# Kernel optimization log

Hardware: AMD Instinct MI355X
Metric: run time of the kernel (lower is better)

Reference implementation:

```python
import jax, jax.numpy as jnp
import numpy as np

LB_WEIGHT = 0.01  # load_balance_loss_weight


def setup_inputs() -> dict:
    key = jax.random.key(0)
    ks = jax.random.split(key, 5)
    B, S, D, F, E = 2, 2048, 1024, 4096, 8
    scale = 0.02
    return {
        "x": jax.random.normal(ks[0], (B, S, D), dtype=jnp.float32),
        "Wr": jax.random.normal(ks[1], (E, D), dtype=jnp.float32) * scale,
        "W1": jax.random.normal(ks[2], (E, F, D), dtype=jnp.float32) * scale,
        "b1": jnp.zeros((E, F), dtype=jnp.float32),
        "W2": jax.random.normal(ks[3], (E, D, F), dtype=jnp.float32) * scale,
        "b2": jnp.zeros((E, D), dtype=jnp.float32),
        "top_k": 2,
    }


def reference(x, Wr, W1, b1, W2, b2, top_k):
    B, S, D = x.shape
    E = Wr.shape[0]
    x_flat = x.reshape(-1, D)                      # (T, D)

    # Router: softmax over experts, then top-k with renormalized gates.
    router_logits = x_flat @ Wr.T                  # (T, E)
    router_probs = jax.nn.softmax(router_logits, axis=-1)
    topk_p, topk_idx = jax.lax.top_k(router_probs, top_k)   # (T, K)
    topk_p = topk_p / jnp.sum(topk_p, axis=-1, keepdims=True)

    # Combine weights per expert: w[t, e] = sum_k topk_p[t, k] * [idx[t, k] == e]
    one_hot = jax.nn.one_hot(topk_idx, E, dtype=x.dtype)     # (T, K, E)
    combine = jnp.einsum("tk,tke->te", topk_p, one_hot)      # (T, E)

    # Expert FFNs (dense over all experts; masked-out experts get zero weight).
    # FeedForward: Linear(D->F) -> GELU -> Linear(F->D); dropout is identity (eval).
    h = jnp.einsum("td,efd->tef", x_flat, W1) + b1           # (T, E, F)
    h = jax.nn.gelu(h)
    expert_out = jnp.einsum("tef,edf->ted", h, W2) + b2      # (T, E, D)

    out_flat = jnp.einsum("te,ted->td", combine, expert_out) # (T, D)
    output = out_flat.reshape(B, S, D)

    # Load-balance aux loss.
    expert_usage = jnp.mean(router_probs, axis=0)            # (E,)
    aux_loss = LB_WEIGHT * jnp.sum((expert_usage - 1.0 / E) ** 2)
    return output, aux_loss
```

## Files before the change

kernel.cpp:

```cpp
#include <hip/hip_runtime.h>
#include <hip/hip_bf16.h>
#include <stdint.h>

#define D_DIM 1024
#define F_DIM 4096
#define E_NUM 8
#define BM2 256
#define BN2 128
#define BK 64
#define MAXTILES 80
#define MAXT256 40

typedef __attribute__((ext_vector_type(4))) float f32x4;
typedef __attribute__((ext_vector_type(8))) short bf16x8;

#define C_CNT   0
#define C_CUR   8
#define C_OFF   16
#define C_NT    25
#define C_TE    26
#define C_TR    (26+MAXTILES)
#define C_USAGE (26+2*MAXTILES)

__device__ __forceinline__ void gload_lds16(const void* g, void* l) {
  __builtin_amdgcn_global_load_lds((const __attribute__((address_space(1))) void*)g,
                                   (__attribute__((address_space(3))) void*)l, 16, 0, 0);
}

__device__ __forceinline__ float bf2f(unsigned short u) {
  union { unsigned int i; float f; } c; c.i = ((unsigned int)u) << 16; return c.f;
}

__global__ void cvt_k(const float* __restrict__ s, unsigned short* __restrict__ d, int n4) {
  const int stride = gridDim.x * blockDim.x;
  for (int i = blockIdx.x * blockDim.x + threadIdx.x; i < n4; i += stride) {
    float4 v = ((const float4*)s)[i];
    __hip_bfloat16 h0 = __float2bfloat16(v.x);
    __hip_bfloat16 h1 = __float2bfloat16(v.y);
    __hip_bfloat16 h2 = __float2bfloat16(v.z);
    __hip_bfloat16 h3 = __float2bfloat16(v.w);
    ushort4 o;
    o.x = *(unsigned short*)&h0; o.y = *(unsigned short*)&h1;
    o.z = *(unsigned short*)&h2; o.w = *(unsigned short*)&h3;
    ((ushort4*)d)[i] = o;
  }
}

__global__ __launch_bounds__(256) void router_k(
    const float* __restrict__ x, const float* __restrict__ Wr,
    int* __restrict__ t2i, float* __restrict__ t2g,
    float* __restrict__ usage_part, unsigned short* __restrict__ xb, int T) {
  __shared__ float us[4][E_NUM];
  const int wave = threadIdx.x >> 6;
  const int lane = threadIdx.x & 63;
  const int gw = blockIdx.x * 4 + wave;
  const float4* xt = (const float4*)(x + (size_t)gw * D_DIM);
  const float4* wr4 = (const float4*)Wr;
  unsigned short* xrow = xb + (size_t)gw * D_DIM;
  float l[E_NUM] = {0.f,0.f,0.f,0.f,0.f,0.f,0.f,0.f};
#pragma unroll
  for (int it = 0; it < D_DIM / 256; it++) {
    const int i4 = it * 64 + lane;
    const float4 xv = xt[i4];
    __hip_bfloat16 c0 = __float2bfloat16(xv.x), c1 = __float2bfloat16(xv.y);
    __hip_bfloat16 c2 = __float2bfloat16(xv.z), c3 = __float2bfloat16(xv.w);
    ushort4 ov; ov.x = *(unsigned short*)&c0; ov.y = *(unsigned short*)&c1;
    ov.z = *(unsigned short*)&c2; ov.w = *(unsigned short*)&c3;
    ((ushort4*)xrow)[i4] = ov;
#pragma unroll
    for (int e = 0; e < E_NUM; e++) {
      const float4 w = wr4[e * (D_DIM / 4) + i4];
      l[e] += xv.x * w.x + xv.y * w.y + xv.z * w.z + xv.w * w.w;
    }
  }
#pragma unroll
  for (int e = 0; e < E_NUM; e++) {
    float v = l[e];
    v += __shfl_xor(v, 32); v += __shfl_xor(v, 16); v += __shfl_xor(v, 8);
    v += __shfl_xor(v, 4);  v += __shfl_xor(v, 2);  v += __shfl_xor(v, 1);
    l[e] = v;
  }
  float m = l[0];
#pragma unroll
  for (int e = 1; e < E_NUM; e++) m = fmaxf(m, l[e]);
  float p[E_NUM]; float s = 0.f;
#pragma unroll
  for (int e = 0; e < E_NUM; e++) { p[e] = expf(l[e] - m); s += p[e]; }
  const float inv = 1.0f / s;
  float v1 = l[0]; int i1 = 0;
#pragma unroll
  for (int e = 1; e < E_NUM; e++) { if (l[e] > v1) { v1 = l[e]; i1 = e; } }
  float v2 = -3.0e38f; int i2 = 0;
#pragma unroll
  for (int e = 0; e < E_NUM; e++) { if (e != i1 && l[e] > v2) { v2 = l[e]; i2 = e; } }
  const float p1 = expf(v1 - m);
  const float p2 = expf(v2 - m);
  const float gd = 1.0f / (p1 + p2);
  if (lane == 0) {
    t2i[gw * 2] = i1; t2i[gw * 2 + 1] = i2;
    t2g[gw * 2] = p1 * gd; t2g[gw * 2 + 1] = p2 * gd;
#pragma unroll
    for (int e = 0; e < E_NUM; e++) us[wave][e] = p[e] * inv;
  }
  __syncthreads();
  if (threadIdx.x < E_NUM) {
    const int e = threadIdx.x;
    usage_part[blockIdx.x * E_NUM + e] = us[0][e] + us[1][e] + us[2][e] + us[3][e];
  }
}

__global__ __launch_bounds__(256) void reduce_k(
    const float* __restrict__ usage_part, const int* __restrict__ t2i,
    int* __restrict__ ctrl, float* __restrict__ aux_out, int nblk, int T2, int T) {
  __shared__ float usum[E_NUM];
  __shared__ int hist[E_NUM];
  if (threadIdx.x < E_NUM) { usum[threadIdx.x] = 0.f; hist[threadIdx.x] = 0; }
  __syncthreads();
  {
    const int e = threadIdx.x & 7;
    const int chunk = threadIdx.x >> 3;
    float s = 0.f;
    for (int i = chunk; i < nblk; i += 32) s += usage_part[i * E_NUM + e];
    atomicAdd(&usum[e], s);
  }
  {
    int h[E_NUM] = {0,0,0,0,0,0,0,0};
    for (int i = threadIdx.x; i < T2; i += 256) h[t2i[i] & 7]++;
#pragma unroll
    for (int e = 0; e < E_NUM; e++) if (h[e]) atomicAdd(&hist[e], h[e]);
  }
  __syncthreads();
  if (threadIdx.x == 0) {
    int off = 0, nt = 0;
    float loss = 0.f;
    for (int e = 0; e < E_NUM; e++) {
      ctrl[C_CNT + e] = hist[e];
      ctrl[C_OFF + e] = off;
      ctrl[C_CUR + e] = off;
      const int c = hist[e];
      const int ntile = (c + BM2 - 1) / BM2;
      for (int i = 0; i < ntile; i++) {
        ctrl[C_TE + nt] = e;
        ctrl[C_TR + nt] = off + i * BM2;
        nt++;
      }
      off += c;
      const float um = usum[e] / (float)T - 1.0f / (float)E_NUM;
      loss += um * um;
    }
    ctrl[C_OFF + E_NUM] = off;
    ctrl[C_NT] = nt;
    aux_out[0] = 0.01f * loss;
  }
}

__global__ void scatter_k(const int* __restrict__ t2i, int* __restrict__ ctrl,
                          int* __restrict__ rmap, int* __restrict__ slots, int T) {
  const int t = blockIdx.x * blockDim.x + threadIdx.x;
  if (t >= T) return;
#pragma unroll
  for (int k = 0; k < 2; k++) {
    const int e = t2i[t * 2 + k];
    const int slot = atomicAdd(&ctrl[C_CUR + e], 1);
    rmap[slot] = t;
    slots[t * 2 + k] = slot;
  }
}


#define STAGE(K0, AL, BL)                                            \
  {                                                                  \
    _Pragma("unroll")                                                \
    for (int i = 0; i < 4; i++) gload_lds16(a_src[i] + (K0), AL[i]); \
    _Pragma("unroll")                                                \
    for (int j = 0; j < 2; j++) gload_lds16(b_src[j] + (K0), BL[j]); \
  }

#define COMPUTE(AC, BC)                                              \
  {                                                                  \
    _Pragma("unroll")                                                \
    for (int kh = 0; kh < 2; ++kh) {                                 \
      const int co = (((kh * 4 + ckq) ^ swz) << 4);                  \
      bf16x8 af[8], bfv[2];                                          \
      _Pragma("unroll")                                              \
      for (int mi = 0; mi < 8; mi++)                                 \
        af[mi] = *(const bf16x8*)((AC) + (rA + mi * 16) * 128 + co); \
      _Pragma("unroll")                                              \
      for (int ni = 0; ni < 2; ni++)                                 \
        bfv[ni] = *(const bf16x8*)((BC) + (rB + ni * 16) * 128 + co);\
      _Pragma("unroll")                                              \
      for (int mi = 0; mi < 8; mi++)                                 \
        _Pragma("unroll")                                            \
        for (int ni = 0; ni < 2; ni++)                               \
          acc[mi][ni] = __builtin_amdgcn_mfma_f32_16x16x32_bf16(af[mi], bfv[ni], acc[mi][ni], 0, 0, 0); \
    }                                                                \
  }

__global__ __launch_bounds__(512, 2) void gemm1_k(
    const unsigned short* __restrict__ xb, const unsigned short* __restrict__ W1b,
    const float* __restrict__ b1, unsigned short* __restrict__ hb,
    const int* __restrict__ rmap, const int* __restrict__ ctrl, int T2) {
  extern __shared__ char smem[];
  const int lin = blockIdx.x;
  const int lin2 = (lin & 7) * 160 + (lin >> 3);
  const int tile = lin2 >> 5;
  const int fbase = (lin2 & 31) * BN2;

  const int nt = ctrl[C_NT];
  if (tile >= nt) return;
  const int e = ctrl[C_TE + tile];
  const int rowbase = ctrl[C_TR + tile];
  const int row_end = ctrl[C_OFF + e + 1];

  const int tid = threadIdx.x;
  const int lane = tid & 63;
  const int wave = tid >> 6;

  const unsigned short* a_src[4];
  const unsigned short* b_src[2];
  char *aL0[4], *aL1[4], *bL0[2], *bL1[2];
#pragma unroll
  for (int i = 0; i < 4; i++) {
    const int c = tid + 512 * i;
    const int r = c >> 3, cc = c & 7;
    const int sc = cc ^ (r & 7);
    int pos = rowbase + r; pos = pos < T2 ? pos : T2 - 1;
    a_src[i] = xb + (size_t)rmap[pos] * D_DIM + sc * 8;
    aL0[i] = smem + c * 16;
    aL1[i] = smem + 32768 + c * 16;
  }
#pragma unroll
  for (int j = 0; j < 2; j++) {
    const int c2 = tid + 512 * j;
    const int r = c2 >> 3, cc = c2 & 7;
    const int sc = cc ^ (r & 7);
    b_src[j] = W1b + ((size_t)e * F_DIM + (size_t)(fbase + r)) * D_DIM + sc * 8;
    bL0[j] = smem + 65536 + c2 * 16;
    bL1[j] = smem + 81920 + c2 * 16;
  }
  const char* As0 = smem;          const char* As1 = smem + 32768;
  const char* Bs0 = smem + 65536;  const char* Bs1 = smem + 81920;

  f32x4 acc[8][2] = {};
  const int wm = wave >> 2, wn = wave & 3;
  const int rA = wm * 128 + (lane & 15);
  const int rB = wn * 32 + (lane & 15);
  const int swz = lane & 7;
  const int ckq = lane >> 4;

  STAGE(0, aL0, bL0);
  const int NK = D_DIM / BK;
  for (int kt = 0; kt < NK; kt += 2) {
    STAGE((kt + 1) * BK, aL1, bL1);
    asm volatile("s_waitcnt vmcnt(6)" ::: "memory");
    __builtin_amdgcn_s_barrier();
    __builtin_amdgcn_sched_barrier(0);
    COMPUTE(As0, Bs0);
    __builtin_amdgcn_sched_barrier(0);
    __builtin_amdgcn_s_barrier();
    if (kt + 2 < NK) {
      STAGE((kt + 2) * BK, aL0, bL0);
      asm volatile("s_waitcnt vmcnt(6)" ::: "memory");
    } else {
      asm volatile("s_waitcnt vmcnt(0)" ::: "memory");
    }
    __builtin_amdgcn_s_barrier();
    __builtin_amdgcn_sched_barrier(0);
    COMPUTE(As1, Bs1);
    __builtin_amdgcn_sched_barrier(0);
    __builtin_amdgcn_s_barrier();
  }

  const int r_rem = row_end - rowbase;
  const float* b1e = b1 + (size_t)e * F_DIM;
  float bias[2];
#pragma unroll
  for (int ni = 0; ni < 2; ni++)
    bias[ni] = b1e[fbase + wn * 32 + ni * 16 + (lane & 15)];
#pragma unroll
  for (int mi = 0; mi < 8; mi++) {
#pragma unroll
    for (int q = 0; q < 4; q++) {
      const int rr = wm * 128 + mi * 16 + (lane >> 4) * 4 + q;
      if (rr < r_rem) {
        unsigned short* hrow = hb + (size_t)(rowbase + rr) * F_DIM;
#pragma unroll
        for (int ni = 0; ni < 2; ni++) {
          const int col = fbase + wn * 32 + ni * 16 + (lane & 15);
          const float v = acc[mi][ni][q] + bias[ni];
          const float u2 = 1.5957691216057308f * (v + 0.044715f * v * v * v);
          const float gg = v / (1.0f + __expf(-u2));
          __hip_bfloat16 hv = __float2bfloat16(gg);
          hrow[col] = *(unsigned short*)&hv;
        }
      }
    }
  }
}

__global__ __launch_bounds__(512, 2) void gemm2_k(
    const unsigned short* __restrict__ hb, const unsigned short* __restrict__ W2b,
    unsigned short* __restrict__ y2, const int* __restrict__ ctrl, int T2) {
  extern __shared__ char smem[];
  const int lin = blockIdx.x;
  const int lin2 = (lin & 7) * 160 + (lin >> 3);
  const int tile = lin2 >> 5;
  const int rest = lin2 & 31;
  const int z = rest >> 3;
  const int dbase = (rest & 7) * BN2;

  const int nt = ctrl[C_NT];
  if (tile >= nt) return;
  const int e = ctrl[C_TE + tile];
  const int rowbase = ctrl[C_TR + tile];
  const int row_end = ctrl[C_OFF + e + 1];
  const int kt0 = z * (F_DIM / BK / 4);

  const int tid = threadIdx.x;
  const int lane = tid & 63;
  const int wave = tid >> 6;

  const unsigned short* a_src[4];
  const unsigned short* b_src[2];
  char *aL0[4], *aL1[4], *bL0[2], *bL1[2];
#pragma unroll
  for (int i = 0; i < 4; i++) {
    const int c = tid + 512 * i;
    const int r = c >> 3, cc = c & 7;
    const int sc = cc ^ (r & 7);
    int pos = rowbase + r; pos = pos < T2 ? pos : T2 - 1;
    a_src[i] = hb + (size_t)pos * F_DIM + sc * 8;
    aL0[i] = smem + c * 16;
    aL1[i] = smem + 32768 + c * 16;
  }
#pragma unroll
  for (int j = 0; j < 2; j++) {
    const int c2 = tid + 512 * j;
    const int r = c2 >> 3, cc = c2 & 7;
    const int sc = cc ^ (r & 7);
    b_src[j] = W2b + ((size_t)e * D_DIM + (size_t)(dbase + r)) * F_DIM + sc * 8;
    bL0[j] = smem + 65536 + c2 * 16;
    bL1[j] = smem + 81920 + c2 * 16;
  }
  const char* As0 = smem;          const char* As1 = smem + 32768;
  const char* Bs0 = smem + 65536;  const char* Bs1 = smem + 81920;

  f32x4 acc[8][2] = {};
  const int wm = wave >> 2, wn = wave & 3;
  const int rA = wm * 128 + (lane & 15);
  const int rB = wn * 32 + (lane & 15);
  const int swz = lane & 7;
  const int ckq = lane >> 4;

  const int NKH = F_DIM / BK / 4;
  STAGE(kt0 * BK, aL0, bL0);
  for (int kt = kt0; kt < kt0 + NKH; kt += 2) {
    STAGE((kt + 1) * BK, aL1, bL1);
    asm volatile("s_waitcnt vmcnt(6)" ::: "memory");
    __builtin_amdgcn_s_barrier();
    __builtin_amdgcn_sched_barrier(0);
    COMPUTE(As0, Bs0);
    __builtin_amdgcn_sched_barrier(0);
    __builtin_amdgcn_s_barrier();
    if (kt + 2 < kt0 + NKH) {
      STAGE((kt + 2) * BK, aL0, bL0);
      asm volatile("s_waitcnt vmcnt(6)" ::: "memory");
    } else {
      asm volatile("s_waitcnt vmcnt(0)" ::: "memory");
    }
    __builtin_amdgcn_s_barrier();
    __builtin_amdgcn_sched_barrier(0);
    COMPUTE(As1, Bs1);
    __builtin_amdgcn_sched_barrier(0);
    __builtin_amdgcn_s_barrier();
  }

  const int r_rem = row_end - rowbase;
  unsigned short* yz = y2 + (size_t)z * T2 * D_DIM;
#pragma unroll
  for (int mi = 0; mi < 8; mi++) {
#pragma unroll
    for (int q = 0; q < 4; q++) {
      const int rr = wm * 128 + mi * 16 + (lane >> 4) * 4 + q;
      if (rr < r_rem) {
        unsigned short* yrow = yz + (size_t)(rowbase + rr) * D_DIM;
#pragma unroll
        for (int ni = 0; ni < 2; ni++) {
          const int col = dbase + wn * 32 + ni * 16 + (lane & 15);
          __hip_bfloat16 hv = __float2bfloat16(acc[mi][ni][q]);
          yrow[col] = *(unsigned short*)&hv;
        }
      }
    }
  }
}

__global__ __launch_bounds__(256) void combine_k(
    const unsigned short* __restrict__ y2, const float* __restrict__ b2,
    const int* __restrict__ t2i, const float* __restrict__ t2g,
    const int* __restrict__ slots, float* __restrict__ out, int T2) {
  const int t = blockIdx.x;
  const int c4 = threadIdx.x;
  const int s0 = slots[t * 2], s1 = slots[t * 2 + 1];
  const int e0 = t2i[t * 2], e1 = t2i[t * 2 + 1];
  const float g0 = t2g[t * 2], g1 = t2g[t * 2 + 1];
  const size_t sl = (size_t)T2 * D_DIM;
  float sum0[4] = {0.f,0.f,0.f,0.f}, sum1[4] = {0.f,0.f,0.f,0.f};
#pragma unroll
  for (int zz = 0; zz < 4; zz++) {
    ushort4 a = ((const ushort4*)(y2 + zz * sl + (size_t)s0 * D_DIM))[c4];
    ushort4 b = ((const ushort4*)(y2 + zz * sl + (size_t)s1 * D_DIM))[c4];
    sum0[0] += bf2f(a.x); sum0[1] += bf2f(a.y); sum0[2] += bf2f(a.z); sum0[3] += bf2f(a.w);
    sum1[0] += bf2f(b.x); sum1[1] += bf2f(b.y); sum1[2] += bf2f(b.z); sum1[3] += bf2f(b.w);
  }
  float4 bb0 = ((const float4*)(b2 + (size_t)e0 * D_DIM))[c4];
  float4 bb1 = ((const float4*)(b2 + (size_t)e1 * D_DIM))[c4];
  float4 o;
  o.x = g0 * (sum0[0] + bb0.x) + g1 * (sum1[0] + bb1.x);
  o.y = g0 * (sum0[1] + bb0.y) + g1 * (sum1[1] + bb1.y);
  o.z = g0 * (sum0[2] + bb0.z) + g1 * (sum1[2] + bb1.z);
  o.w = g0 * (sum0[3] + bb0.w) + g1 * (sum1[3] + bb1.w);
  ((float4*)(out + (size_t)t * D_DIM))[c4] = o;
}

extern "C" void kernel_launch(void* const* d_in, const int* in_sizes, int n_in,
                              void* d_out, int out_size, void* d_ws, size_t ws_size,
                              hipStream_t stream) {
  const float* x  = (const float*)d_in[0];
  const float* Wr = (const float*)d_in[1];
  const float* W1 = (const float*)d_in[2];
  const float* b1 = (const float*)d_in[3];
  const float* W2 = (const float*)d_in[4];
  const float* b2 = (const float*)d_in[5];
  float* out = (float*)d_out;

  const int T = in_sizes[0] / D_DIM;
  const int T2 = T * 2;
  const int nblk = T / 4;

  char* ws = (char*)d_ws;
  size_t o = 0;
  unsigned short* xb  = (unsigned short*)(ws + o); o += (size_t)T * D_DIM * 2;
  unsigned short* W1b = (unsigned short*)(ws + o); o += (size_t)E_NUM * F_DIM * D_DIM * 2;
  unsigned short* W2b = (unsigned short*)(ws + o); o += (size_t)E_NUM * D_DIM * F_DIM * 2;
  unsigned short* hb  = (unsigned short*)(ws + o); o += (size_t)T2 * F_DIM * 2;
  int*   ctrl  = (int*)(ws + o);   o += 4096;
  int*   t2i   = (int*)(ws + o);   o += (size_t)T2 * 4;
  float* t2g   = (float*)(ws + o); o += (size_t)T2 * 4;
  int*   rmap  = (int*)(ws + o);   o += (size_t)T2 * 4;
  int*   slots = (int*)(ws + o);   o += (size_t)T2 * 4;
  float* usage_part = (float*)(ws + o); o += (size_t)nblk * E_NUM * 4;
  unsigned short* y2 = W1b;

  hipFuncSetAttribute((const void*)gemm1_k, hipFuncAttributeMaxDynamicSharedMemorySize, 98304);
  hipFuncSetAttribute((const void*)gemm2_k, hipFuncAttributeMaxDynamicSharedMemorySize, 98304);

  hipMemsetAsync(ctrl, 0, 4096, stream);

  cvt_k<<<1024, 256, 0, stream>>>(W1, W1b, E_NUM * F_DIM * D_DIM / 4);
  cvt_k<<<1024, 256, 0, stream>>>(W2, W2b, E_NUM * D_DIM * F_DIM / 4);

  router_k<<<nblk, 256, 0, stream>>>(x, Wr, t2i, t2g, usage_part, xb, T);
  reduce_k<<<1, 256, 0, stream>>>(usage_part, t2i, ctrl, out + (size_t)(out_size - 1), nblk, T2, T);
  scatter_k<<<(T + 255) / 256, 256, 0, stream>>>(t2i, ctrl, rmap, slots, T);

  gemm1_k<<<MAXT256 * 32, 512, 98304, stream>>>(xb, W1b, b1, hb, rmap, ctrl, T2);
  gemm2_k<<<MAXT256 * 32, 512, 98304, stream>>>(hb, W2b, y2, ctrl, T2);
  combine_k<<<T, 256, 0, stream>>>(y2, b2, t2i, t2g, slots, out, T2);
}
```

Baseline: 377.3 us.

## Fuse fp32-to-bf16 weight conversion into expert GEMM tile loads

Drops the two standalone conversion kernels that turned W1 and W2 from fp32 to bf16 on every call. The expert GEMMs now stage fp32 weight tiles straight into LDS with a 16-chunk XOR swizzle and convert each B fragment to bf16 in registers before the MFMA. This saves a full read and write pass over both weight tensors. In exchange, each GEMM reads twice the weight bytes per tile, adds VALU conversion work in the inner loop, and raises dynamic LDS to 128 KB per block, which can lower how many blocks fit on a CU. The y2 scratch buffer, which used to reuse the W1b space, gets its own workspace region.

```diff
diff --git a/kernel.cpp b/kernel.cpp
--- a/kernel.cpp
+++ b/kernel.cpp
@@ -31,19 +31,9 @@
   union { unsigned int i; float f; } c; c.i = ((unsigned int)u) << 16; return c.f;
 }
 
-__global__ void cvt_k(const float* __restrict__ s, unsigned short* __restrict__ d, int n4) {
-  const int stride = gridDim.x * blockDim.x;
-  for (int i = blockIdx.x * blockDim.x + threadIdx.x; i < n4; i += stride) {
-    float4 v = ((const float4*)s)[i];
-    __hip_bfloat16 h0 = __float2bfloat16(v.x);
-    __hip_bfloat16 h1 = __float2bfloat16(v.y);
-    __hip_bfloat16 h2 = __float2bfloat16(v.z);
-    __hip_bfloat16 h3 = __float2bfloat16(v.w);
-    ushort4 o;
-    o.x = *(unsigned short*)&h0; o.y = *(unsigned short*)&h1;
-    o.z = *(unsigned short*)&h2; o.w = *(unsigned short*)&h3;
-    ((ushort4*)d)[i] = o;
-  }
+__device__ __forceinline__ short bfs(float f) {
+  __hip_bfloat16 h = __float2bfloat16(f);
+  return *(short*)&h;
 }
 
 __global__ __launch_bounds__(256) void router_k(
@@ -168,15 +158,15 @@
 }
 
 
-#define STAGE(K0, AL, BL)                                            \
+#define STAGEF(K0, AL, BL)                                           \
   {                                                                  \
     _Pragma("unroll")                                                \
     for (int i = 0; i < 4; i++) gload_lds16(a_src[i] + (K0), AL[i]); \
     _Pragma("unroll")                                                \
-    for (int j = 0; j < 2; j++) gload_lds16(b_src[j] + (K0), BL[j]); \
-  }
-
-#define COMPUTE(AC, BC)                                              \
+    for (int j = 0; j < 4; j++) gload_lds16(b_srcF[j] + (K0), BL[j]);\
+  }
+
+#define COMPUTEF(AC, BC)                                             \
   {                                                                  \
     _Pragma("unroll")                                                \
     for (int kh = 0; kh < 2; ++kh) {                                 \
@@ -186,8 +176,17 @@
       for (int mi = 0; mi < 8; mi++)                                 \
         af[mi] = *(const bf16x8*)((AC) + (rA + mi * 16) * 128 + co); \
       _Pragma("unroll")                                              \
-      for (int ni = 0; ni < 2; ni++)                                 \
-        bfv[ni] = *(const bf16x8*)((BC) + (rB + ni * 16) * 128 + co);\
+      for (int ni = 0; ni < 2; ni++) {                               \
+        const int row = rB + ni * 16;                                \
+        const int cka = ((kh * 8 + ckq * 2) ^ swzB) << 4;            \
+        const int ckb = ((kh * 8 + ckq * 2 + 1) ^ swzB) << 4;        \
+        const float4 fa = *(const float4*)((BC) + row * 256 + cka);  \
+        const float4 fb = *(const float4*)((BC) + row * 256 + ckb);  \
+        bf16x8 w;                                                    \
+        w[0] = bfs(fa.x); w[1] = bfs(fa.y); w[2] = bfs(fa.z); w[3] = bfs(fa.w); \
+        w[4] = bfs(fb.x); w[5] = bfs(fb.y); w[6] = bfs(fb.z); w[7] = bfs(fb.w); \
+        bfv[ni] = w;                                                 \
+      }                                                              \
       _Pragma("unroll")                                              \
       for (int mi = 0; mi < 8; mi++)                                 \
         _Pragma("unroll")                                            \
@@ -197,7 +196,7 @@
   }
 
 __global__ __launch_bounds__(512, 2) void gemm1_k(
-    const unsigned short* __restrict__ xb, const unsigned short* __restrict__ W1b,
+    const unsigned short* __restrict__ xb, const float* __restrict__ W1,
     const float* __restrict__ b1, unsigned short* __restrict__ hb,
     const int* __restrict__ rmap, const int* __restrict__ ctrl, int T2) {
   extern __shared__ char smem[];
@@ -217,8 +216,8 @@
   const int wave = tid >> 6;
 
   const unsigned short* a_src[4];
-  const unsigned short* b_src[2];
-  char *aL0[4], *aL1[4], *bL0[2], *bL1[2];
+  const float* b_srcF[4];
+  char *aL0[4], *aL1[4], *bL0[4], *bL1[4];
 #pragma unroll
   for (int i = 0; i < 4; i++) {
     const int c = tid + 512 * i;
@@ -230,43 +229,44 @@
     aL1[i] = smem + 32768 + c * 16;
   }
 #pragma unroll
-  for (int j = 0; j < 2; j++) {
+  for (int j = 0; j < 4; j++) {
     const int c2 = tid + 512 * j;
-    const int r = c2 >> 3, cc = c2 & 7;
-    const int sc = cc ^ (r & 7);
-    b_src[j] = W1b + ((size_t)e * F_DIM + (size_t)(fbase + r)) * D_DIM + sc * 8;
+    const int r = c2 >> 4, cc16 = c2 & 15;
+    const int sc16 = cc16 ^ (r & 15);
+    b_srcF[j] = W1 + ((size_t)e * F_DIM + (size_t)(fbase + r)) * D_DIM + sc16 * 4;
     bL0[j] = smem + 65536 + c2 * 16;
-    bL1[j] = smem + 81920 + c2 * 16;
+    bL1[j] = smem + 98304 + c2 * 16;
   }
   const char* As0 = smem;          const char* As1 = smem + 32768;
-  const char* Bs0 = smem + 65536;  const char* Bs1 = smem + 81920;
+  const char* Bs0 = smem + 65536;  const char* Bs1 = smem + 98304;
 
   f32x4 acc[8][2] = {};
   const int wm = wave >> 2, wn = wave & 3;
   const int rA = wm * 128 + (lane & 15);
   const int rB = wn * 32 + (lane & 15);
   const int swz = lane & 7;
+  const int swzB = lane & 15;
   const int ckq = lane >> 4;
 
-  STAGE(0, aL0, bL0);
+  STAGEF(0, aL0, bL0);
   const int NK = D_DIM / BK;
   for (int kt = 0; kt < NK; kt += 2) {
-    STAGE((kt + 1) * BK, aL1, bL1);
-    asm volatile("s_waitcnt vmcnt(6)" ::: "memory");
-    __builtin_amdgcn_s_barrier();
-    __builtin_amdgcn_sched_barrier(0);
-    COMPUTE(As0, Bs0);
+    STAGEF((kt + 1) * BK, aL1, bL1);
+    asm volatile("s_waitcnt vmcnt(8)" ::: "memory");
+    __builtin_amdgcn_s_barrier();
+    __builtin_amdgcn_sched_barrier(0);
+    COMPUTEF(As0, Bs0);
     __builtin_amdgcn_sched_barrier(0);
     __builtin_amdgcn_s_barrier();
     if (kt + 2 < NK) {
-      STAGE((kt + 2) * BK, aL0, bL0);
-      asm volatile("s_waitcnt vmcnt(6)" ::: "memory");
+      STAGEF((kt + 2) * BK, aL0, bL0);
+      asm volatile("s_waitcnt vmcnt(8)" ::: "memory");
     } else {
       asm volatile("s_waitcnt vmcnt(0)" ::: "memory");
     }
     __builtin_amdgcn_s_barrier();
     __builtin_amdgcn_sched_barrier(0);
-    COMPUTE(As1, Bs1);
+    COMPUTEF(As1, Bs1);
     __builtin_amdgcn_sched_barrier(0);
     __builtin_amdgcn_s_barrier();
   }
@@ -299,7 +299,7 @@
 }
 
 __global__ __launch_bounds__(512, 2) void gemm2_k(
-    const unsigned short* __restrict__ hb, const unsigned short* __restrict__ W2b,
+    const unsigned short* __restrict__ hb, const float* __restrict__ W2,
     unsigned short* __restrict__ y2, const int* __restrict__ ctrl, int T2) {
   extern __shared__ char smem[];
   const int lin = blockIdx.x;
@@ -321,8 +321,8 @@
   const int wave = tid >> 6;
 
   const unsigned short* a_src[4];
-  const unsigned short* b_src[2];
-  char *aL0[4], *aL1[4], *bL0[2], *bL1[2];
+  const float* b_srcF[4];
+  char *aL0[4], *aL1[4], *bL0[4], *bL1[4];
 #pragma unroll
   for (int i = 0; i < 4; i++) {
     const int c = tid + 512 * i;
@@ -334,43 +334,44 @@
     aL1[i] = smem + 32768 + c * 16;
   }
 #pragma unroll
-  for (int j = 0; j < 2; j++) {
+  for (int j = 0; j < 4; j++) {
     const int c2 = tid + 512 * j;
-    const int r = c2 >> 3, cc = c2 & 7;
-    const int sc = cc ^ (r & 7);
-    b_src[j] = W2b + ((size_t)e * D_DIM + (size_t)(dbase + r)) * F_DIM + sc * 8;
+    const int r = c2 >> 4, cc16 = c2 & 15;
+    const int sc16 = cc16 ^ (r & 15);
+    b_srcF[j] = W2 + ((size_t)e * D_DIM + (size_t)(dbase + r)) * F_DIM + sc16 * 4;
     bL0[j] = smem + 65536 + c2 * 16;
-    bL1[j] = smem + 81920 + c2 * 16;
+    bL1[j] = smem + 98304 + c2 * 16;
   }
   const char* As0 = smem;          const char* As1 = smem + 32768;
-  const char* Bs0 = smem + 65536;  const char* Bs1 = smem + 81920;
+  const char* Bs0 = smem + 65536;  const char* Bs1 = smem + 98304;
 
   f32x4 acc[8][2] = {};
   const int wm = wave >> 2, wn = wave & 3;
   const int rA = wm * 128 + (lane & 15);
   const int rB = wn * 32 + (lane & 15);
   const int swz = lane & 7;
+  const int swzB = lane & 15;
   const int ckq = lane >> 4;
 
   const int NKH = F_DIM / BK / 4;
-  STAGE(kt0 * BK, aL0, bL0);
+  STAGEF(kt0 * BK, aL0, bL0);
   for (int kt = kt0; kt < kt0 + NKH; kt += 2) {
-    STAGE((kt + 1) * BK, aL1, bL1);
-    asm volatile("s_waitcnt vmcnt(6)" ::: "memory");
-    __builtin_amdgcn_s_barrier();
-    __builtin_amdgcn_sched_barrier(0);
-    COMPUTE(As0, Bs0);
+    STAGEF((kt + 1) * BK, aL1, bL1);
+    asm volatile("s_waitcnt vmcnt(8)" ::: "memory");
+    __builtin_amdgcn_s_barrier();
+    __builtin_amdgcn_sched_barrier(0);
+    COMPUTEF(As0, Bs0);
     __builtin_amdgcn_sched_barrier(0);
     __builtin_amdgcn_s_barrier();
     if (kt + 2 < kt0 + NKH) {
-      STAGE((kt + 2) * BK, aL0, bL0);
-      asm volatile("s_waitcnt vmcnt(6)" ::: "memory");
+      STAGEF((kt + 2) * BK, aL0, bL0);
+      asm volatile("s_waitcnt vmcnt(8)" ::: "memory");
     } else {
       asm volatile("s_waitcnt vmcnt(0)" ::: "memory");
     }
     __builtin_amdgcn_s_barrier();
     __builtin_amdgcn_sched_barrier(0);
-    COMPUTE(As1, Bs1);
+    COMPUTEF(As1, Bs1);
     __builtin_amdgcn_sched_barrier(0);
     __builtin_amdgcn_s_barrier();
   }
@@ -441,30 +442,25 @@
   char* ws = (char*)d_ws;
   size_t o = 0;
   unsigned short* xb  = (unsigned short*)(ws + o); o += (size_t)T * D_DIM * 2;
-  unsigned short* W1b = (unsigned short*)(ws + o); o += (size_t)E_NUM * F_DIM * D_DIM * 2;
-  unsigned short* W2b = (unsigned short*)(ws + o); o += (size_t)E_NUM * D_DIM * F_DIM * 2;
   unsigned short* hb  = (unsigned short*)(ws + o); o += (size_t)T2 * F_DIM * 2;
+  unsigned short* y2  = (unsigned short*)(ws + o); o += (size_t)4 * T2 * D_DIM * 2;
   int*   ctrl  = (int*)(ws + o);   o += 4096;
   int*   t2i   = (int*)(ws + o);   o += (size_t)T2 * 4;
   float* t2g   = (float*)(ws + o); o += (size_t)T2 * 4;
   int*   rmap  = (int*)(ws + o);   o += (size_t)T2 * 4;
   int*   slots = (int*)(ws + o);   o += (size_t)T2 * 4;
   float* usage_part = (float*)(ws + o); o += (size_t)nblk * E_NUM * 4;
-  unsigned short* y2 = W1b;
-
-  hipFuncSetAttribute((const void*)gemm1_k, hipFuncAttributeMaxDynamicSharedMemorySize, 98304);
-  hipFuncSetAttribute((const void*)gemm2_k, hipFuncAttributeMaxDynamicSharedMemorySize, 98304);
+
+  hipFuncSetAttribute((const void*)gemm1_k, hipFuncAttributeMaxDynamicSharedMemorySize, 131072);
+  hipFuncSetAttribute((const void*)gemm2_k, hipFuncAttributeMaxDynamicSharedMemorySize, 131072);
 
   hipMemsetAsync(ctrl, 0, 4096, stream);
-
-  cvt_k<<<1024, 256, 0, stream>>>(W1, W1b, E_NUM * F_DIM * D_DIM / 4);
-  cvt_k<<<1024, 256, 0, stream>>>(W2, W2b, E_NUM * D_DIM * F_DIM / 4);
 
   router_k<<<nblk, 256, 0, stream>>>(x, Wr, t2i, t2g, usage_part, xb, T);
   reduce_k<<<1, 256, 0, stream>>>(usage_part, t2i, ctrl, out + (size_t)(out_size - 1), nblk, T2, T);
   scatter_k<<<(T + 255) / 256, 256, 0, stream>>>(t2i, ctrl, rmap, slots, T);
 
-  gemm1_k<<<MAXT256 * 32, 512, 98304, stream>>>(xb, W1b, b1, hb, rmap, ctrl, T2);
-  gemm2_k<<<MAXT256 * 32, 512, 98304, stream>>>(hb, W2b, y2, ctrl, T2);
+  gemm1_k<<<MAXT256 * 32, 512, 131072, stream>>>(xb, W1, b1, hb, rmap, ctrl, T2);
+  gemm2_k<<<MAXT256 * 32, 512, 131072, stream>>>(hb, W2, y2, ctrl, T2);
   combine_k<<<T, 256, 0, stream>>>(y2, b2, t2i, t2g, slots, out, T2);
 }
```

Result: slower. 473.8 us (+25.6%).
